# Performance work log

Hardware: AMD Instinct MI355X
Metric: run time of the kernel (lower is better)

The kernel has to match this reference:

```python
import jax, jax.numpy as jnp
import numpy as np

N_EMBD = 1024
N_HEAD = 16
HEAD_DIM = N_EMBD // N_HEAD
SEQ = 2048
BATCH = 2
WINDOW = 256
SCALE = 1.0 / np.sqrt(HEAD_DIM)
MASK_VALUE = -10000.0


def setup_inputs() -> dict:
    key = jax.random.key(0)
    ks = jax.random.split(key, 5)
    s = 0.02
    return {
        "hidden_states": jax.random.normal(ks[0], (BATCH, SEQ, N_EMBD), dtype=jnp.float32),
        "w_attn": jax.random.normal(ks[1], (N_EMBD, 3 * N_EMBD), dtype=jnp.float32) * s,
        "b_attn": jnp.zeros((3 * N_EMBD,), dtype=jnp.float32),
        "w_proj": jax.random.normal(ks[2], (N_EMBD, N_EMBD), dtype=jnp.float32) * s,
        "b_proj": jnp.zeros((N_EMBD,), dtype=jnp.float32),
    }


def _mask(seq_len):
    # causal AND sliding window: j <= i and j > i - WINDOW
    i = jnp.arange(seq_len)[:, None]
    j = jnp.arange(seq_len)[None, :]
    return (j <= i) & (j > i - WINDOW)  # [T, T] bool


def reference(hidden_states, w_attn, b_attn, w_proj, b_proj):
    B, T, _ = hidden_states.shape
    qkv = hidden_states @ w_attn + b_attn  # [B, T, 3E]
    q, k, v = jnp.split(qkv, 3, axis=-1)
    # [B, H, T, D]
    q = q.reshape(B, T, N_HEAD, HEAD_DIM).transpose(0, 2, 1, 3)
    k = k.reshape(B, T, N_HEAD, HEAD_DIM).transpose(0, 2, 1, 3)
    v = v.reshape(B, T, N_HEAD, HEAD_DIM).transpose(0, 2, 1, 3)

    scores = jnp.einsum("bhqd,bhkd->bhqk", q, k) * SCALE  # [B, H, T, T]
    mask = _mask(T)[None, None]  # [1, 1, T, T]
    scores = jnp.where(mask, scores, MASK_VALUE)
    scores = jnp.clip(scores, -10000.0, 10000.0)
    attn = jax.nn.softmax(scores, axis=-1)
    out = jnp.einsum("bhqk,bhkd->bhqd", attn, v)  # [B, H, T, D]
    out = out.transpose(0, 2, 1, 3).reshape(B, T, N_EMBD)
    return out @ w_proj + b_proj
```

## Files before the change

kernel.cpp:

```cpp
#include <hip/hip_runtime.h>


typedef __bf16 bf16_t;
typedef bf16_t bf16x8 __attribute__((ext_vector_type(8)));
typedef bf16_t bf16x4 __attribute__((ext_vector_type(4)));
typedef float  floatx4 __attribute__((ext_vector_type(4)));

#define SEQ_T   2048
#define NHEAD   16
#define HDIM    64
#define EMB     1024
#define WIN     256
#define SCALE_F 0.125f

__device__ __forceinline__ int detect_bf16(const uint4* __restrict__ det)
{
    const int lane = threadIdx.x & 63;
    const uint4 v = det[lane];
    int c = 0;
    #pragma unroll
    for (int e = 0; e < 4; ++e) {
        const unsigned int ex = ((&v.x)[e] >> 7) & 0xffu;
        c += (ex >= 100u && ex <= 150u) ? 1 : 0;
    }
    #pragma unroll
    for (int m = 32; m >= 1; m >>= 1) c += __shfl_xor(c, m, 64);
    return (c * 2 > 256) ? 1 : 0;
}

__global__ __launch_bounds__(256) void prologue(
    const void* __restrict__ hidden, bf16_t* __restrict__ Hc,
    const void* __restrict__ ba, bf16_t* __restrict__ bba,
    const void* __restrict__ bp, bf16_t* __restrict__ bbp,
    const void* __restrict__ wA, bf16_t* __restrict__ WtA,
    const void* __restrict__ wP, bf16_t* __restrict__ WtP)
{
    __shared__ __align__(16) bf16_t tile[64][68];
    const int f = detect_bf16((const uint4*)hidden);
    const int blk = blockIdx.x;

    if (blk < 4100) {
        if (f) return;
        const float* src;
        bf16_t* dst;
        int base;
        if (blk < 4096)      { src = (const float*)hidden; dst = Hc;  base = blk * 1024; }
        else if (blk < 4099) { src = (const float*)ba;     dst = bba; base = (blk - 4096) * 1024; }
        else                 { src = (const float*)bp;     dst = bbp; base = 0; }
        const int i4 = base + threadIdx.x * 4;
        const float4 x = *(const float4*)(src + i4);
        bf16x4 v;
        v[0] = (bf16_t)x.x; v[1] = (bf16_t)x.y;
        v[2] = (bf16_t)x.z; v[3] = (bf16_t)x.w;
        *(bf16x4*)(dst + i4) = v;
        return;
    }

    int id = blk - 4100;
    const void* W; bf16_t* Wt; int N, bx, by;
    if (id < 768) { W = wA; Wt = WtA; N = 3072; bx = id % 48; by = id / 48; }
    else { id -= 768; W = wP; Wt = WtP; N = 1024; bx = id % 16; by = id / 16; }
    const int K = 1024;
    const int n0 = bx * 64;
    const int k0 = by * 64;
    const int tx = threadIdx.x & 15;
    const int ty = threadIdx.x >> 4;

    #pragma unroll
    for (int r = ty; r < 64; r += 16) {
        bf16x4 v;
        const size_t base = (size_t)(k0 + r) * N + n0 + tx * 4;
        if (f) {
            v = *(const bf16x4*)((const bf16_t*)W + base);
        } else {
            const float4 x = *(const float4*)((const float*)W + base);
            v[0] = (bf16_t)x.x; v[1] = (bf16_t)x.y;
            v[2] = (bf16_t)x.z; v[3] = (bf16_t)x.w;
        }
        *(bf16x4*)&tile[r][tx * 4] = v;
    }
    __syncthreads();
    #pragma unroll
    for (int r = ty; r < 64; r += 16) {
        bf16x4 v;
        v[0] = tile[tx * 4 + 0][r];
        v[1] = tile[tx * 4 + 1][r];
        v[2] = tile[tx * 4 + 2][r];
        v[3] = tile[tx * 4 + 3][r];
        *(bf16x4*)(Wt + (size_t)(n0 + r) * K + k0 + tx * 4) = v;
    }
}

template<int BNt>
__global__ __launch_bounds__(256, 2) void gemm_bt_bias(
    const bf16_t* __restrict__ Abf,
    const bf16_t* __restrict__ Aalt,
    const bf16_t* __restrict__ Bt,
    const bf16_t* __restrict__ biasbf,
    const bf16_t* __restrict__ biasalt,
    void* __restrict__ C,
    int M, int N, int K,
    int force_bf16, const uint4* __restrict__ det)
{
    constexpr int BMt = 128;
    constexpr int NF  = BNt / 32;
    __shared__ __align__(16) bf16_t As[BMt * 64];
    __shared__ __align__(16) bf16_t Bs[BNt * 64];

    const int flag = detect_bf16(det);
    const bf16_t* A    = flag ? Abf    : Aalt;
    const bf16_t* bias = flag ? biasbf : biasalt;
    const int obf = force_bf16 | flag;

    const int tid  = threadIdx.x;
    const int wave = tid >> 6;
    const int lane = tid & 63;
    const int quad = lane >> 4;
    const int n16  = lane & 15;
    const int m0 = blockIdx.y * BMt;
    const int n0 = blockIdx.x * BNt;
    const int wm = (wave >> 1) * 64;
    const int wn = (wave & 1) * (BNt / 2);

    floatx4 acc[4][NF] = {};

    const int lr = lane >> 3;
    const int g8 = ((lane & 7) ^ lr) * 8;

    for (int k0 = 0; k0 < K; k0 += 64) {
        #pragma unroll
        for (int t = 0; t < BMt / 32; ++t) {
            const int row0 = wave * (BMt / 4) + t * 8;
            const bf16_t* ga = A + (size_t)(m0 + row0 + lr) * K + k0 + g8;
            __builtin_amdgcn_global_load_lds(
                (const __attribute__((address_space(1))) void*)ga,
                (__attribute__((address_space(3))) void*)(As + row0 * 64),
                16, 0, 0);
        }
        #pragma unroll
        for (int t = 0; t < BNt / 32; ++t) {
            const int row0 = wave * (BNt / 4) + t * 8;
            const bf16_t* gb = Bt + (size_t)(n0 + row0 + lr) * K + k0 + g8;
            __builtin_amdgcn_global_load_lds(
                (const __attribute__((address_space(1))) void*)gb,
                (__attribute__((address_space(3))) void*)(Bs + row0 * 64),
                16, 0, 0);
        }
        __syncthreads();

        #pragma unroll
        for (int s = 0; s < 2; ++s) {
            const int ch = (((4 * s + quad) ^ (n16 & 7)) * 8);
            const bf16_t* pa = As + (wm + n16) * 64 + ch;
            const bf16_t* pb = Bs + (wn + n16) * 64 + ch;
            bf16x8 af[4], bfr[NF];
            #pragma unroll
            for (int ff = 0; ff < 4; ++ff)
                af[ff] = *(const bf16x8*)(pa + ff * 16 * 64);
            #pragma unroll
            for (int ff = 0; ff < NF; ++ff)
                bfr[ff] = *(const bf16x8*)(pb + ff * 16 * 64);
            #pragma unroll
            for (int mf = 0; mf < 4; ++mf)
                #pragma unroll
                for (int nf = 0; nf < NF; ++nf)
                    acc[mf][nf] = __builtin_amdgcn_mfma_f32_16x16x32_bf16(
                        af[mf], bfr[nf], acc[mf][nf], 0, 0, 0);
        }
        __syncthreads();
    }

    const int col   = n0 + wn + n16;
    const int rbase = m0 + wm + quad * 4;
    #pragma unroll
    for (int nf = 0; nf < NF; ++nf) {
        const float bv = (float)bias[col + nf * 16];
        #pragma unroll
        for (int mf = 0; mf < 4; ++mf) {
            #pragma unroll
            for (int r = 0; r < 4; ++r) {
                const size_t idx =
                    (size_t)(rbase + mf * 16 + r) * N + col + nf * 16;
                const float val = acc[mf][nf][r] + bv;
                if (obf) ((bf16_t*)C)[idx] = (bf16_t)val;
                else     ((float*)C)[idx]  = val;
            }
        }
    }
}

#define CW   160
#define VT_S 168
#define P_S  168

__global__ __launch_bounds__(256) void attn_mfma(
    const bf16_t* __restrict__ qkv,
    bf16_t* __restrict__ attn_out)
{
    __shared__ __align__(16) bf16_t Ks[CW * 64];
    __shared__ __align__(16) bf16_t Vt[64 * VT_S];
    __shared__ __align__(16) bf16_t Pst[4][16 * P_S];

    const int tid  = threadIdx.x;
    const int wave = tid >> 6;
    const int lane = tid & 63;
    const int quad = lane >> 4;
    const int n16  = lane & 15;

    const int i0 = blockIdx.x * 64;
    const int h  = blockIdx.y;
    const int b  = blockIdx.z;
    const size_t rowbase = (size_t)b * SEQ_T;
    const int kbase  = i0 - 256;
    const int iw     = 16 * wave;
    const int climit = 256 - i0;

    const bf16_t* Qg = qkv + (rowbase + i0 + iw + n16) * (3 * EMB) + h * HDIM;
    bf16x8 qf[2];
    qf[0] = *(const bf16x8*)(Qg + quad * 8);
    qf[1] = *(const bf16x8*)(Qg + 32 + quad * 8);

    floatx4 Oac[4] = {};
    float m_run[4], l_run[4];
    #pragma unroll
    for (int rr = 0; rr < 4; ++rr) { m_run[rr] = -3.0e38f; l_run[rr] = 0.f; }

    for (int hc = 0; hc < 2; ++hc) {
        const int cbase = hc * CW;

        bf16x8 vreg[5];
        #pragma unroll
        for (int t = 0; t < 5; ++t) {
            const int idx = tid + 256 * t;
            const int lc  = idx >> 3;
            const int d0  = (idx & 7) * 8;
            int j = kbase + cbase + lc; if (j < 0) j = 0;
            vreg[t] = *(const bf16x8*)(qkv + (rowbase + j) * (3 * EMB)
                                       + 2 * EMB + h * HDIM + d0);
        }

        __syncthreads();

        #pragma unroll
        for (int t = 0; t < 5; ++t) {
            const int lc0 = wave * 40 + t * 8;
            const int lcL = lc0 + (lane >> 3);
            int j = kbase + cbase + lcL; if (j < 0) j = 0;
            const int g = (lane & 7) ^ (lcL & 7);
            const bf16_t* src = qkv + (rowbase + j) * (3 * EMB)
                                + EMB + h * HDIM + g * 8;
            __builtin_amdgcn_global_load_lds(
                (const __attribute__((address_space(1))) void*)src,
                (__attribute__((address_space(3))) void*)(Ks + lc0 * 64),
                16, 0, 0);
        }

        #pragma unroll
        for (int t = 0; t < 5; ++t) {
            const int idx = tid + 256 * t;
            const int lc  = idx >> 3;
            const int d0  = (idx & 7) * 8;
            #pragma unroll
            for (int e = 0; e < 8; ++e)
                Vt[(d0 + e) * VT_S + lc] = vreg[t][e];
        }

        __syncthreads();

        floatx4 sc[10];
        #pragma unroll
        for (int tt = 0; tt < 10; ++tt) {
            sc[tt] = (floatx4){0.f, 0.f, 0.f, 0.f};
            #pragma unroll
            for (int s2 = 0; s2 < 2; ++s2) {
                const int lc = 16 * tt + n16;
                const int ch = (4 * s2 + quad) ^ (lc & 7);
                const bf16x8 kf = *(const bf16x8*)(Ks + lc * 64 + ch * 8);
                sc[tt] = __builtin_amdgcn_mfma_f32_16x16x32_bf16(
                    qf[s2], kf, sc[tt], 0, 0, 0);
            }
        }

        #pragma unroll
        for (int tt = 0; tt < 10; ++tt) {
            const int c  = cbase + 16 * tt + n16;
            const int cw = c - iw;
            #pragma unroll
            for (int rr = 0; rr < 4; ++rr) {
                const int r = quad * 4 + rr;
                const bool valid = (cw > r) && (cw <= r + 256) && (c >= climit);
                sc[tt][rr] = valid ? sc[tt][rr] * SCALE_F : -3.0e38f;
            }
        }

        float cm[4];
        #pragma unroll
        for (int rr = 0; rr < 4; ++rr) {
            cm[rr] = -3.0e38f;
            #pragma unroll
            for (int tt = 0; tt < 10; ++tt) cm[rr] = fmaxf(cm[rr], sc[tt][rr]);
            #pragma unroll
            for (int m = 8; m >= 1; m >>= 1)
                cm[rr] = fmaxf(cm[rr], __shfl_xor(cm[rr], m, 64));
        }

        #pragma unroll
        for (int rr = 0; rr < 4; ++rr) {
            const float mnew  = fmaxf(m_run[rr], cm[rr]);
            const float alpha = __expf(m_run[rr] - mnew);
            m_run[rr] = mnew;
            l_run[rr] *= alpha;
            #pragma unroll
            for (int nt = 0; nt < 4; ++nt) Oac[nt][rr] *= alpha;
        }

        float psum[4] = {0.f, 0.f, 0.f, 0.f};
        #pragma unroll
        for (int tt = 0; tt < 10; ++tt) {
            #pragma unroll
            for (int rr = 0; rr < 4; ++rr) {
                const float s = sc[tt][rr];
                const float e = (s > -1.0e38f) ? __expf(s - m_run[rr]) : 0.f;
                psum[rr] += e;
                Pst[wave][(quad * 4 + rr) * P_S + 16 * tt + n16] = (bf16_t)e;
            }
        }
        #pragma unroll
        for (int rr = 0; rr < 4; ++rr) {
            #pragma unroll
            for (int m = 8; m >= 1; m >>= 1)
                psum[rr] += __shfl_xor(psum[rr], m, 64);
            l_run[rr] += psum[rr];
        }

        __syncthreads();

        #pragma unroll
        for (int ks = 0; ks < 5; ++ks) {
            const bf16x8 paf = *(const bf16x8*)(
                &Pst[wave][n16 * P_S + ks * 32 + quad * 8]);
            #pragma unroll
            for (int nt = 0; nt < 4; ++nt) {
                const bf16x8 vbf = *(const bf16x8*)(
                    Vt + (nt * 16 + n16) * VT_S + ks * 32 + quad * 8);
                Oac[nt] = __builtin_amdgcn_mfma_f32_16x16x32_bf16(
                    paf, vbf, Oac[nt], 0, 0, 0);
            }
        }
    }

    #pragma unroll
    for (int rr = 0; rr < 4; ++rr) {
        const float rden = 1.0f / l_run[rr];
        const size_t row = rowbase + i0 + iw + quad * 4 + rr;
        #pragma unroll
        for (int nt = 0; nt < 4; ++nt) {
            attn_out[row * EMB + h * HDIM + nt * 16 + n16] =
                (bf16_t)(Oac[nt][rr] * rden);
        }
    }
}

extern "C" void kernel_launch(void* const* d_in, const int* in_sizes, int n_in,
                              void* d_out, int out_size, void* d_ws, size_t ws_size,
                              hipStream_t stream)
{
    const void* hidden = d_in[0];
    const void* w_attn = d_in[1];
    const void* b_attn = d_in[2];
    const void* w_proj = d_in[3];
    const void* b_proj = d_in[4];

    char* ws = (char*)d_ws;
    bf16_t* Wt_attn = (bf16_t*)(ws);
    bf16_t* Wt_proj = (bf16_t*)(ws + (6u << 20));
    bf16_t* qkv     = (bf16_t*)(ws + (8u << 20));
    bf16_t* attn_o  = (bf16_t*)(ws + (32u << 20));
    bf16_t* Hc      = (bf16_t*)(ws + (40u << 20));
    bf16_t* bb_attn = (bf16_t*)(ws + (48u << 20));
    bf16_t* bb_proj = (bf16_t*)(ws + (48u << 20) + 8192);

    const uint4* det = (const uint4*)hidden;

    prologue<<<5124, 256, 0, stream>>>(hidden, Hc, b_attn, bb_attn,
                                       b_proj, bb_proj,
                                       w_attn, Wt_attn, w_proj, Wt_proj);

    gemm_bt_bias<256><<<dim3(3072 / 256, 4096 / 128), 256, 0, stream>>>(
        (const bf16_t*)hidden, Hc, Wt_attn,
        (const bf16_t*)b_attn, bb_attn, qkv, 4096, 3072, 1024, 1, det);

    attn_mfma<<<dim3(SEQ_T / 64, NHEAD, 2), 256, 0, stream>>>(qkv, attn_o);

    gemm_bt_bias<64><<<dim3(1024 / 64, 4096 / 128), 256, 0, stream>>>(
        attn_o, attn_o, Wt_proj,
        (const bf16_t*)b_proj, bb_proj, (void*)d_out, 4096, 1024, 1024, 0, det);
}
```

Before: 172.1 us.

## Pipeline attention K/V staging in smaller chunks and widen proj GEMM K tile

The attention kernel now walks the key window in four chunks of 80 instead of two of 160. It prefetches the next chunk's V into registers and issues the next K async load to LDS while the current chunk's softmax and PV MFMAs run, so global-memory latency overlaps compute. The padded tail of the Vt and P tiles is zero-filled so the third 32-wide k-step reads zeros. The GEMM is templated on its K tile, and the output projection uses a 128-deep tile to halve loop iterations and barriers, at the cost of more LDS per block and possibly lower occupancy.

Result: faster. 168.5 us (-2.1%).

```diff
diff --git a/kernel.cpp b/kernel.cpp
--- a/kernel.cpp
+++ b/kernel.cpp
@@ -91,7 +91,7 @@
     }
 }
 
-template<int BNt>
+template<int BNt, int BKt>
 __global__ __launch_bounds__(256, 2) void gemm_bt_bias(
     const bf16_t* __restrict__ Abf,
     const bf16_t* __restrict__ Aalt,
@@ -104,8 +104,12 @@
 {
     constexpr int BMt = 128;
     constexpr int NF  = BNt / 32;
-    __shared__ __align__(16) bf16_t As[BMt * 64];
-    __shared__ __align__(16) bf16_t Bs[BNt * 64];
+    constexpr int LPR = BKt / 8;
+    constexpr int CM  = LPR - 1;
+    constexpr int RPL = 64 / LPR;
+    constexpr int SL  = BKt / 32;
+    __shared__ __align__(16) bf16_t As[BMt * BKt];
+    __shared__ __align__(16) bf16_t Bs[BNt * BKt];
 
     const int flag = detect_bf16(det);
     const bf16_t* A    = flag ? Abf    : Aalt;
@@ -124,42 +128,44 @@
 
     floatx4 acc[4][NF] = {};
 
-    const int lr = lane >> 3;
-    const int g8 = ((lane & 7) ^ lr) * 8;
-
-    for (int k0 = 0; k0 < K; k0 += 64) {
-        #pragma unroll
-        for (int t = 0; t < BMt / 32; ++t) {
-            const int row0 = wave * (BMt / 4) + t * 8;
-            const bf16_t* ga = A + (size_t)(m0 + row0 + lr) * K + k0 + g8;
+    const int lr   = lane / LPR;
+    const int lc16 = lane % LPR;
+
+    for (int k0 = 0; k0 < K; k0 += BKt) {
+        #pragma unroll
+        for (int t = 0; t < (BMt / 4) / RPL; ++t) {
+            const int row0 = wave * (BMt / 4) + t * RPL;
+            const int g = (lc16 ^ ((row0 + lr) & CM)) * 8;
+            const bf16_t* ga = A + (size_t)(m0 + row0 + lr) * K + k0 + g;
             __builtin_amdgcn_global_load_lds(
                 (const __attribute__((address_space(1))) void*)ga,
-                (__attribute__((address_space(3))) void*)(As + row0 * 64),
+                (__attribute__((address_space(3))) void*)(As + row0 * BKt),
                 16, 0, 0);
         }
         #pragma unroll
-        for (int t = 0; t < BNt / 32; ++t) {
-            const int row0 = wave * (BNt / 4) + t * 8;
-            const bf16_t* gb = Bt + (size_t)(n0 + row0 + lr) * K + k0 + g8;
+        for (int t = 0; t < (BNt / 4) / RPL; ++t) {
+            const int row0 = wave * (BNt / 4) + t * RPL;
+            const int g = (lc16 ^ ((row0 + lr) & CM)) * 8;
+            const bf16_t* gb = Bt + (size_t)(n0 + row0 + lr) * K + k0 + g;
             __builtin_amdgcn_global_load_lds(
                 (const __attribute__((address_space(1))) void*)gb,
-                (__attribute__((address_space(3))) void*)(Bs + row0 * 64),
+                (__attribute__((address_space(3))) void*)(Bs + row0 * BKt),
                 16, 0, 0);
         }
         __syncthreads();
 
         #pragma unroll
-        for (int s = 0; s < 2; ++s) {
-            const int ch = (((4 * s + quad) ^ (n16 & 7)) * 8);
-            const bf16_t* pa = As + (wm + n16) * 64 + ch;
-            const bf16_t* pb = Bs + (wn + n16) * 64 + ch;
+        for (int s = 0; s < SL; ++s) {
+            const int ch = (((4 * s + quad) ^ (n16 & CM)) * 8);
+            const bf16_t* pa = As + (wm + n16) * BKt + ch;
+            const bf16_t* pb = Bs + (wn + n16) * BKt + ch;
             bf16x8 af[4], bfr[NF];
             #pragma unroll
             for (int ff = 0; ff < 4; ++ff)
-                af[ff] = *(const bf16x8*)(pa + ff * 16 * 64);
+                af[ff] = *(const bf16x8*)(pa + ff * 16 * BKt);
             #pragma unroll
             for (int ff = 0; ff < NF; ++ff)
-                bfr[ff] = *(const bf16x8*)(pb + ff * 16 * 64);
+                bfr[ff] = *(const bf16x8*)(pb + ff * 16 * BKt);
             #pragma unroll
             for (int mf = 0; mf < 4; ++mf)
                 #pragma unroll
@@ -189,9 +195,10 @@
     }
 }
 
-#define CW   160
-#define VT_S 168
-#define P_S  168
+#define CW   80
+#define NCH  4
+#define VT_S 104
+#define P_S  104
 
 __global__ __launch_bounds__(256) void attn_mfma(
     const bf16_t* __restrict__ qkv,
@@ -220,33 +227,39 @@
     qf[0] = *(const bf16x8*)(Qg + quad * 8);
     qf[1] = *(const bf16x8*)(Qg + 32 + quad * 8);
 
+    for (int i = tid; i < 1024; i += 256)
+        Vt[(i >> 4) * VT_S + 80 + (i & 15)] = (bf16_t)0.f;
+    for (int i = tid; i < 1024; i += 256)
+        Pst[i >> 8][((i >> 4) & 15) * P_S + 80 + (i & 15)] = (bf16_t)0.f;
+
     floatx4 Oac[4] = {};
     float m_run[4], l_run[4];
     #pragma unroll
     for (int rr = 0; rr < 4; ++rr) { m_run[rr] = -3.0e38f; l_run[rr] = 0.f; }
 
-    for (int hc = 0; hc < 2; ++hc) {
+    bf16x8 vreg[3];
+
+    auto loadV = [&](int hc) {
         const int cbase = hc * CW;
-
-        bf16x8 vreg[5];
-        #pragma unroll
-        for (int t = 0; t < 5; ++t) {
+        #pragma unroll
+        for (int t = 0; t < 3; ++t) {
             const int idx = tid + 256 * t;
-            const int lc  = idx >> 3;
-            const int d0  = (idx & 7) * 8;
-            int j = kbase + cbase + lc; if (j < 0) j = 0;
-            vreg[t] = *(const bf16x8*)(qkv + (rowbase + j) * (3 * EMB)
-                                       + 2 * EMB + h * HDIM + d0);
-        }
-
-        __syncthreads();
-
-        #pragma unroll
-        for (int t = 0; t < 5; ++t) {
-            const int lc0 = wave * 40 + t * 8;
+            if (idx < 640) {
+                const int lc = idx >> 3;
+                const int d0 = (idx & 7) * 8;
+                int j = kbase + cbase + lc; if (j < 0) j = 0;
+                vreg[t] = *(const bf16x8*)(qkv + (rowbase + j) * (3 * EMB)
+                                           + 2 * EMB + h * HDIM + d0);
+            }
+        }
+    };
+    auto stageK = [&](int hc) {
+        const int cbase = hc * CW;
+        for (int t = wave; t < 10; t += 4) {
+            const int lc0 = t * 8;
             const int lcL = lc0 + (lane >> 3);
             int j = kbase + cbase + lcL; if (j < 0) j = 0;
-            const int g = (lane & 7) ^ (lcL & 7);
+            const int g = (lane & 7) ^ (lane >> 3);
             const bf16_t* src = qkv + (rowbase + j) * (3 * EMB)
                                 + EMB + h * HDIM + g * 8;
             __builtin_amdgcn_global_load_lds(
@@ -254,22 +267,36 @@
                 (__attribute__((address_space(3))) void*)(Ks + lc0 * 64),
                 16, 0, 0);
         }
-
-        #pragma unroll
-        for (int t = 0; t < 5; ++t) {
+    };
+    auto writeVt = [&]() {
+        #pragma unroll
+        for (int t = 0; t < 3; ++t) {
             const int idx = tid + 256 * t;
-            const int lc  = idx >> 3;
-            const int d0  = (idx & 7) * 8;
-            #pragma unroll
-            for (int e = 0; e < 8; ++e)
-                Vt[(d0 + e) * VT_S + lc] = vreg[t][e];
-        }
+            if (idx < 640) {
+                const int lc = idx >> 3;
+                const int d0 = (idx & 7) * 8;
+                #pragma unroll
+                for (int e = 0; e < 8; ++e)
+                    Vt[(d0 + e) * VT_S + lc] = vreg[t][e];
+            }
+        }
+    };
+
+    loadV(0);
+    stageK(0);
+
+    for (int hc = 0; hc < NCH; ++hc) {
+        const int cbase = hc * CW;
 
         __syncthreads();
-
-        floatx4 sc[10];
-        #pragma unroll
-        for (int tt = 0; tt < 10; ++tt) {
+        writeVt();
+        __syncthreads();
+
+        if (hc < NCH - 1) loadV(hc + 1);
+
+        floatx4 sc[5];
+        #pragma unroll
+        for (int tt = 0; tt < 5; ++tt) {
             sc[tt] = (floatx4){0.f, 0.f, 0.f, 0.f};
             #pragma unroll
             for (int s2 = 0; s2 < 2; ++s2) {
@@ -282,7 +309,7 @@
         }
 
         #pragma unroll
-        for (int tt = 0; tt < 10; ++tt) {
+        for (int tt = 0; tt < 5; ++tt) {
             const int c  = cbase + 16 * tt + n16;
             const int cw = c - iw;
             #pragma unroll
@@ -298,12 +325,11 @@
         for (int rr = 0; rr < 4; ++rr) {
             cm[rr] = -3.0e38f;
             #pragma unroll
-            for (int tt = 0; tt < 10; ++tt) cm[rr] = fmaxf(cm[rr], sc[tt][rr]);
+            for (int tt = 0; tt < 5; ++tt) cm[rr] = fmaxf(cm[rr], sc[tt][rr]);
             #pragma unroll
             for (int m = 8; m >= 1; m >>= 1)
                 cm[rr] = fmaxf(cm[rr], __shfl_xor(cm[rr], m, 64));
         }
-
         #pragma unroll
         for (int rr = 0; rr < 4; ++rr) {
             const float mnew  = fmaxf(m_run[rr], cm[rr]);
@@ -316,7 +342,7 @@
 
         float psum[4] = {0.f, 0.f, 0.f, 0.f};
         #pragma unroll
-        for (int tt = 0; tt < 10; ++tt) {
+        for (int tt = 0; tt < 5; ++tt) {
             #pragma unroll
             for (int rr = 0; rr < 4; ++rr) {
                 const float s = sc[tt][rr];
@@ -335,8 +361,10 @@
 
         __syncthreads();
 
-        #pragma unroll
-        for (int ks = 0; ks < 5; ++ks) {
+        if (hc < NCH - 1) stageK(hc + 1);
+
+        #pragma unroll
+        for (int ks = 0; ks < 3; ++ks) {
             const bf16x8 paf = *(const bf16x8*)(
                 &Pst[wave][n16 * P_S + ks * 32 + quad * 8]);
             #pragma unroll
@@ -386,13 +414,13 @@
                                        b_proj, bb_proj,
                                        w_attn, Wt_attn, w_proj, Wt_proj);
 
-    gemm_bt_bias<256><<<dim3(3072 / 256, 4096 / 128), 256, 0, stream>>>(
+    gemm_bt_bias<256, 64><<<dim3(3072 / 256, 4096 / 128), 256, 0, stream>>>(
         (const bf16_t*)hidden, Hc, Wt_attn,
         (const bf16_t*)b_attn, bb_attn, qkv, 4096, 3072, 1024, 1, det);
 
     attn_mfma<<<dim3(SEQ_T / 64, NHEAD, 2), 256, 0, stream>>>(qkv, attn_o);
 
-    gemm_bt_bias<64><<<dim3(1024 / 64, 4096 / 128), 256, 0, stream>>>(
+    gemm_bt_bias<64, 128><<<dim3(1024 / 64, 4096 / 128), 256, 0, stream>>>(
         attn_o, attn_o, Wt_proj,
         (const bf16_t*)b_proj, bb_proj, (void*)d_out, 4096, 1024, 1024, 0, det);
 }
```
